# Performance work log

Hardware: AMD Instinct MI355X
Metric: run time of the kernel (lower is better)

Reference implementation:

```python
import jax, jax.numpy as jnp
import numpy as np

L = 21          # number of kernel positions
C0, C1 = 32, 32 # kernel_channels
IN_DIM = 7      # 3 + 3 + 1 geometric features


def leaky_relu(x):
    return jnp.where(x >= 0, x, 0.2 * x)


def setup_inputs() -> dict:
    key = jax.random.key(0)
    k1, k2, k3, k4, k5 = jax.random.split(key, 5)
    E = 1_000_000
    inp = jax.random.normal(k1, (E, IN_DIM), dtype=jnp.float32)
    idx = jax.random.randint(k2, (E,), 0, L, dtype=jnp.int32)
    # kaiming-uniform style init for Ws, zeros for bs (per reset_parameters)
    def ku(k, shape):
        fan = shape[1] * shape[2]
        gain = np.sqrt(2.0 / (1 + np.sqrt(5) ** 2))
        bound = np.sqrt(3.0) * gain / np.sqrt(fan)
        return jax.random.uniform(k, shape, jnp.float32, -bound, bound)
    W0 = ku(k3, (L, IN_DIM, C0))
    b0 = jnp.zeros((L, C0), dtype=jnp.float32)
    W1 = ku(k4, (L, C0, C1))
    b1 = jnp.zeros((L, C1), dtype=jnp.float32)
    return {"input": inp, "idx": idx, "W0": W0, "b0": b0, "W1": W1, "b1": b1}


def reference(input, idx, W0, b0, W1, b1):
    # layer 0: gather per-edge [7, C0] weight, 1x7 @ 7xC0 matmul, bias, leaky-relu
    h = leaky_relu(jnp.einsum('ek,ekc->ec', input, W0[idx]) + b0[idx])
    # layer 1: gather per-edge [C0, C1] weight
    w = leaky_relu(jnp.einsum('ek,ekc->ec', h, W1[idx]) + b1[idx])
    return w
```

## Files before the change

### kernel.cpp

```cpp
#include <hip/hip_runtime.h>

#define L 21
#define C0 32
#define C1 32
#define IN_DIM 7
#define GHIST 256
#define BPAD 256

__global__ __launch_bounds__(256) void k_hist(const int* __restrict__ idx, int E,
                                              int* __restrict__ blockCounts) {
  __shared__ int h[L];
  int tid = threadIdx.x;
  if (tid < L) h[tid] = 0;
  __syncthreads();
  int per = (E + GHIST - 1) / GHIST;
  int s = blockIdx.x * per;
  int e = min(E, s + per);
  for (int i = s + tid; i < e; i += blockDim.x)
    atomicAdd(&h[idx[i]], 1);
  __syncthreads();
  if (tid < L) blockCounts[blockIdx.x * L + tid] = h[tid];
}

__global__ __launch_bounds__(256) void k_scan(const int* __restrict__ blockCounts,
                                              int* __restrict__ cursor,
                                              int* __restrict__ endArr,
                                              int* __restrict__ baseArr) {
  __shared__ int tot[L];
  __shared__ int base[L + 1];
  int tid = threadIdx.x;
  if (tid < L) {
    int s = 0;
#pragma unroll 8
    for (int b = 0; b < GHIST; b++) s += blockCounts[b * L + tid];
    tot[tid] = s;
  }
  __syncthreads();
  if (tid == 0) {
    int a = 0;
    for (int l = 0; l < L; l++) { base[l] = a; a += (tot[l] + BPAD - 1) & ~(BPAD - 1); }
    base[L] = a;
  }
  __syncthreads();
  if (tid < L) {
    int a = base[tid];
#pragma unroll 8
    for (int b = 0; b < GHIST; b++) {
      cursor[b * L + tid] = a;
      a += blockCounts[b * L + tid];
    }
    endArr[tid] = base[tid] + tot[tid];
  }
  if (tid <= L) baseArr[tid] = base[tid];
}

__global__ __launch_bounds__(256) void k_scatter(const int* __restrict__ idx,
                                                 const float* __restrict__ inp, int E,
                                                 const int* __restrict__ cursor,
                                                 int* __restrict__ perm,
                                                 float* __restrict__ xb) {
  __shared__ int cur[L];
  int tid = threadIdx.x;
  if (tid < L) cur[tid] = cursor[blockIdx.x * L + tid];
  __syncthreads();
  int per = (E + GHIST - 1) / GHIST;
  int s = blockIdx.x * per;
  int e = min(E, s + per);
  for (int i = s + tid; i < e; i += blockDim.x) {
    int l = idx[i];
    int pos = atomicAdd(&cur[l], 1);
    perm[pos] = i;
    const float* row = inp + (size_t)i * IN_DIM;
    float4 a, b;
    a.x = row[0]; a.y = row[1]; a.z = row[2]; a.w = row[3];
    b.x = row[4]; b.y = row[5]; b.z = row[6]; b.w = 0.f;
    float4* dst = (float4*)(xb + (size_t)pos * 8);
    dst[0] = a;
    dst[1] = b;
  }
}

template <bool USE_XB>
__global__ __launch_bounds__(256) void k_compute(const float* __restrict__ xb,
                                                 const float* __restrict__ inp,
                                                 const float* __restrict__ W0g,
                                                 const float* __restrict__ b0g,
                                                 const float* __restrict__ W1g,
                                                 const float* __restrict__ b1g,
                                                 const int* __restrict__ perm,
                                                 const int* __restrict__ baseArr,
                                                 const int* __restrict__ endArr,
                                                 float* __restrict__ out) {
  int T = threadIdx.x;
  int lane = T & 63;
  int blockbase = blockIdx.x << 8;

  int bv = baseArr[lane <= L ? lane : L];
  unsigned long long m = __ballot((lane <= L) && (blockbase >= bv));
  int l = __popcll(m) - 1;
  if (l >= L) return;
  l = __builtin_amdgcn_readfirstlane(l);
  int end = __builtin_amdgcn_readfirstlane(endArr[l]);

  int slot = blockbase + T;

  float x[IN_DIM];
  if (USE_XB) {
    const float4* xrow = (const float4*)(xb + (size_t)slot * 8);
    float4 xa = xrow[0], xc = xrow[1];
    x[0] = xa.x; x[1] = xa.y; x[2] = xa.z; x[3] = xa.w;
    x[4] = xc.x; x[5] = xc.y; x[6] = xc.z;
  } else {
    int p0 = slot < end ? perm[slot] : 0;
    const float* row = inp + (size_t)p0 * IN_DIM;
#pragma unroll
    for (int k = 0; k < IN_DIM; k++) x[k] = row[k];
  }

  const float* w0 = W0g + l * (IN_DIM * C0);
  const float* B0 = b0g + l * C0;
  const float* w1 = W1g + l * (C0 * C1);
  const float* B1 = b1g + l * C1;

  float h[C0];
#pragma unroll
  for (int c = 0; c < C0; c++) h[c] = B0[c];
#pragma unroll
  for (int k = 0; k < IN_DIM; k++) {
#pragma unroll
    for (int c = 0; c < C0; c++) h[c] = fmaf(x[k], w0[k * C0 + c], h[c]);
  }
#pragma unroll
  for (int c = 0; c < C0; c++) h[c] = h[c] >= 0.f ? h[c] : 0.2f * h[c];

  float o[C1];
#pragma unroll
  for (int c = 0; c < C1; c++) o[c] = B1[c];
#pragma unroll
  for (int k = 0; k < C0; k++) {
#pragma unroll
    for (int c = 0; c < C1; c++) o[c] = fmaf(h[k], w1[k * C1 + c], o[c]);
  }
#pragma unroll
  for (int c = 0; c < C1; c++) o[c] = o[c] >= 0.f ? o[c] : 0.2f * o[c];

  __shared__ float obuf[4 * 64 * 32];
  float* tile = &obuf[(T >> 6) * (64 * 32)];
#pragma unroll
  for (int cq = 0; cq < 32; cq += 4) {
    int ad = lane * 32 + (cq ^ ((lane & 7) << 2));
    float4 v = {o[cq], o[cq + 1], o[cq + 2], o[cq + 3]};
    *(float4*)&tile[ad] = v;
  }
  int wavebase = blockbase + (T >> 6) * 64;
  int q = (lane & 7) * 4;
  int rbase = lane >> 3;
#pragma unroll
  for (int step = 0; step < 8; step++) {
    int row = step * 8 + rbase;
    int slot_r = wavebase + row;
    if (slot_r < end) {
      int p = perm[slot_r];
      int sw = (row & 7) << 2;
      float4 v = *(const float4*)&tile[row * 32 + (q ^ sw)];
      *(float4*)(out + (size_t)p * C1 + q) = v;
    }
  }
}

extern "C" void kernel_launch(void* const* d_in, const int* in_sizes, int n_in,
                              void* d_out, int out_size, void* d_ws, size_t ws_size,
                              hipStream_t stream) {
  const float* inp = (const float*)d_in[0];
  const int* idx   = (const int*)d_in[1];
  const float* W0  = (const float*)d_in[2];
  const float* b0  = (const float*)d_in[3];
  const float* W1  = (const float*)d_in[4];
  const float* b1  = (const float*)d_in[5];
  float* out = (float*)d_out;
  int E = in_sizes[1];

  int nBlk = (E + 255) / 256 + L;
  size_t slots = (size_t)nBlk * 256;

  int* ws = (int*)d_ws;
  int* blockCounts = ws;
  int* cursor      = blockCounts + GHIST * L;
  int* endArr      = cursor + GHIST * L;
  int* baseArr     = endArr + L;
  int* perm        = baseArr + (L + 1);
  size_t ints = (size_t)2 * GHIST * L + L + (L + 1) + slots;
  ints = (ints + 3) & ~(size_t)3;
  float* xb = (float*)(ws + ints);
  size_t need = ints * 4 + slots * 8 * 4;
  bool use_xb = ws_size >= need;

  k_hist<<<GHIST, 256, 0, stream>>>(idx, E, blockCounts);
  k_scan<<<1, 256, 0, stream>>>(blockCounts, cursor, endArr, baseArr);
  k_scatter<<<GHIST, 256, 0, stream>>>(idx, inp, E, cursor, perm, xb);

  if (use_xb) {
    k_compute<true><<<nBlk, 256, 0, stream>>>(xb, inp, W0, b0, W1, b1,
                                              perm, baseArr, endArr, out);
  } else {
    k_compute<false><<<nBlk, 256, 0, stream>>>(nullptr, inp, W0, b0, W1, b1,
                                               perm, baseArr, endArr, out);
  }
}
```

Baseline: 87.42 us.

## Write sorted outputs contiguously to scratch, then gather back via rank

Compute now writes its results contiguously into a sorted-order scratch buffer instead of scattering them through perm. A new k_out kernel then gathers each edge's row using a rank array recorded during scatter, so writes to the output are coalesced. The change replaces scattered 128-byte row writes with an extra pass: a full 128 MB write plus read of scratch, a rank array, and one more launch. The fallback path without the xb buffer is removed, so mode 1 still reads xb even when the workspace is too small for it.

```diff
diff --git a/kernel.cpp b/kernel.cpp
--- a/kernel.cpp
+++ b/kernel.cpp
@@ -58,6 +58,7 @@
                                                  const float* __restrict__ inp, int E,
                                                  const int* __restrict__ cursor,
                                                  int* __restrict__ perm,
+                                                 int* __restrict__ rank,
                                                  float* __restrict__ xb) {
   __shared__ int cur[L];
   int tid = threadIdx.x;
@@ -70,6 +71,7 @@
     int l = idx[i];
     int pos = atomicAdd(&cur[l], 1);
     perm[pos] = i;
+    rank[i] = pos;
     const float* row = inp + (size_t)i * IN_DIM;
     float4 a, b;
     a.x = row[0]; a.y = row[1]; a.z = row[2]; a.w = row[3];
@@ -80,9 +82,8 @@
   }
 }
 
-template <bool USE_XB>
+template <int MODE>
 __global__ __launch_bounds__(256) void k_compute(const float* __restrict__ xb,
-                                                 const float* __restrict__ inp,
                                                  const float* __restrict__ W0g,
                                                  const float* __restrict__ b0g,
                                                  const float* __restrict__ W1g,
@@ -90,7 +91,7 @@
                                                  const int* __restrict__ perm,
                                                  const int* __restrict__ baseArr,
                                                  const int* __restrict__ endArr,
-                                                 float* __restrict__ out) {
+                                                 float* __restrict__ dstbuf) {
   int T = threadIdx.x;
   int lane = T & 63;
   int blockbase = blockIdx.x << 8;
@@ -104,18 +105,9 @@
 
   int slot = blockbase + T;
 
-  float x[IN_DIM];
-  if (USE_XB) {
-    const float4* xrow = (const float4*)(xb + (size_t)slot * 8);
-    float4 xa = xrow[0], xc = xrow[1];
-    x[0] = xa.x; x[1] = xa.y; x[2] = xa.z; x[3] = xa.w;
-    x[4] = xc.x; x[5] = xc.y; x[6] = xc.z;
-  } else {
-    int p0 = slot < end ? perm[slot] : 0;
-    const float* row = inp + (size_t)p0 * IN_DIM;
-#pragma unroll
-    for (int k = 0; k < IN_DIM; k++) x[k] = row[k];
-  }
+  const float4* xrow = (const float4*)(xb + (size_t)slot * 8);
+  float4 xa = xrow[0], xc = xrow[1];
+  float x[IN_DIM] = {xa.x, xa.y, xa.z, xa.w, xc.x, xc.y, xc.z};
 
   const float* w0 = W0g + l * (IN_DIM * C0);
   const float* B0 = b0g + l * C0;
@@ -159,11 +151,30 @@
   for (int step = 0; step < 8; step++) {
     int row = step * 8 + rbase;
     int slot_r = wavebase + row;
-    if (slot_r < end) {
+    int sw = (row & 7) << 2;
+    float4 v = *(const float4*)&tile[row * 32 + (q ^ sw)];
+    if (MODE == 2) {
+      *(float4*)(dstbuf + (size_t)slot_r * C1 + q) = v;
+    } else if (slot_r < end) {
       int p = perm[slot_r];
-      int sw = (row & 7) << 2;
-      float4 v = *(const float4*)&tile[row * 32 + (q ^ sw)];
-      *(float4*)(out + (size_t)p * C1 + q) = v;
+      *(float4*)(dstbuf + (size_t)p * C1 + q) = v;
+    }
+  }
+}
+
+__global__ __launch_bounds__(256) void k_out(const float* __restrict__ scratch,
+                                             const int* __restrict__ rank,
+                                             float* __restrict__ out, int E) {
+  int T = threadIdx.x;
+  int base = blockIdx.x << 8;
+  int q = (T & 7) * 4;
+#pragma unroll
+  for (int j = 0; j < 8; j++) {
+    int e = base + j * 32 + (T >> 3);
+    if (e < E) {
+      int r = rank[e];
+      float4 v = *(const float4*)(scratch + (size_t)r * C1 + q);
+      *(float4*)(out + (size_t)e * C1 + q) = v;
     }
   }
 }
@@ -189,21 +200,25 @@
   int* endArr      = cursor + GHIST * L;
   int* baseArr     = endArr + L;
   int* perm        = baseArr + (L + 1);
-  size_t ints = (size_t)2 * GHIST * L + L + (L + 1) + slots;
+  int* rank        = perm + slots;
+  size_t ints = (size_t)2 * GHIST * L + L + (L + 1) + slots + E;
   ints = (ints + 3) & ~(size_t)3;
   float* xb = (float*)(ws + ints);
-  size_t need = ints * 4 + slots * 8 * 4;
-  bool use_xb = ws_size >= need;
+  float* scratch = xb + slots * 8;
+  size_t need1 = ints * 4 + slots * 8 * 4;
+  size_t need2 = need1 + slots * 32 * 4;
+  int mode = ws_size >= need2 ? 2 : (ws_size >= need1 ? 1 : 1);
 
   k_hist<<<GHIST, 256, 0, stream>>>(idx, E, blockCounts);
   k_scan<<<1, 256, 0, stream>>>(blockCounts, cursor, endArr, baseArr);
-  k_scatter<<<GHIST, 256, 0, stream>>>(idx, inp, E, cursor, perm, xb);
-
-  if (use_xb) {
-    k_compute<true><<<nBlk, 256, 0, stream>>>(xb, inp, W0, b0, W1, b1,
-                                              perm, baseArr, endArr, out);
+  k_scatter<<<GHIST, 256, 0, stream>>>(idx, inp, E, cursor, perm, rank, xb);
+
+  if (mode == 2) {
+    k_compute<2><<<nBlk, 256, 0, stream>>>(xb, W0, b0, W1, b1,
+                                           perm, baseArr, endArr, scratch);
+    k_out<<<(E + 255) / 256, 256, 0, stream>>>(scratch, rank, out, E);
   } else {
-    k_compute<false><<<nBlk, 256, 0, stream>>>(nullptr, inp, W0, b0, W1, b1,
-                                               perm, baseArr, endArr, out);
-  }
-}
+    k_compute<1><<<nBlk, 256, 0, stream>>>(xb, W0, b0, W1, b1,
+                                           perm, baseArr, endArr, out);
+  }
+}
```

Result: slower. 165.7 us (+89.5%).
